# Kernel tuning notes

Measured on AMD Instinct MI355X. Metric: run time of the kernel, lower is better.

Reference implementation:

```python
import jax, jax.numpy as jnp
import numpy as np

NUM_EMBEDDINGS = 8192
EMBEDDING_DIM = 256
BETA = 0.25


def setup_inputs() -> dict:
    key = jax.random.key(0)
    k1, k2 = jax.random.split(key)
    z = jax.random.normal(k1, (16, 256, 32, 32), dtype=jnp.float32)
    # torch init: uniform(-1/K, 1/K)
    emb_w = jax.random.uniform(k2, (NUM_EMBEDDINGS, EMBEDDING_DIM),
                               dtype=jnp.float32,
                               minval=-1.0 / NUM_EMBEDDINGS,
                               maxval=1.0 / NUM_EMBEDDINGS)
    return {"z": z, "emb_w": emb_w}


def reference(z, emb_w):
    B, C, H, W = z.shape
    z_bhwc = jnp.transpose(z, (0, 2, 3, 1))          # [B,H,W,C]
    flat = z_bhwc.reshape(-1, C)                      # [N,C]
    d = (jnp.sum(flat * flat, axis=1, keepdims=True)
         + jnp.sum(emb_w * emb_w, axis=1)
         - 2.0 * flat @ emb_w.T)                      # [N,K]
    idx = jnp.argmin(d, axis=1)                       # [N]
    # direct gather (mathematically identical to one-hot @ emb_w)
    quantized = emb_w[idx].reshape(z_bhwc.shape)      # [B,H,W,C]
    q_latent_loss = jnp.mean((jax.lax.stop_gradient(quantized) - z_bhwc) ** 2)
    e_latent_loss = jnp.mean((quantized - jax.lax.stop_gradient(z_bhwc)) ** 2)
    loss = q_latent_loss + BETA * e_latent_loss
    # straight-through estimator
    quantized_st = z_bhwc + jax.lax.stop_gradient(quantized - z_bhwc)
    out = jnp.transpose(quantized_st, (0, 3, 1, 2))   # [B,C,H,W]
    return out, loss, idx.reshape(B, -1)
```

## Files before the change

### kernel.cpp

```cpp
#include <hip/hip_runtime.h>
#include <cstdint>
#include <cstddef>

#define N_PIX   16384
#define K_EMB   8192
#define DDIM    256

#define WS_A8       0
#define WS_E8       4194304
#define WS_KEYS     6291456
#define WS_ZSQ      23068672
#define WS_ESQ      23134208
#define WS_LOSS     23166976
#define WS_CNT      23166984

typedef float f32x16 __attribute__((ext_vector_type(16)));
typedef int   i32x4  __attribute__((ext_vector_type(4)));
typedef int   i32x8  __attribute__((ext_vector_type(8)));

__device__ __forceinline__ unsigned int f32_sortable(float f) {
    unsigned int u = __float_as_uint(f);
    return (u & 0x80000000u) ? ~u : (u | 0x80000000u);
}

__device__ __forceinline__ unsigned char f2fp8(float x) {
    unsigned ub = __float_as_uint(x);
    unsigned sgn = (ub >> 24) & 0x80u;
    unsigned b = ub & 0x7FFFFFFFu;
    unsigned out;
    if (__uint_as_float(b) < 0.015625f) {
        out = (unsigned)(int)rintf(__uint_as_float(b) * 512.0f);
    } else {
        unsigned r = b + 0x7FFFFu + ((b >> 20) & 1u);
        int er = (int)(r >> 23) - 127;
        out = (unsigned)(((er + 7) << 3) | ((r >> 20) & 7u));
    }
    return (unsigned char)(out | sgn);
}

#if defined(__has_builtin)
#if __has_builtin(__builtin_amdgcn_cvt_pk_fp8_f32)
#define HAVE_CVT_FP8 1
#endif
#if __has_builtin(__builtin_amdgcn_fmed3f)
#define HAVE_FMED3 1
#endif
#endif

__device__ __forceinline__ unsigned pack4_fp8(float a, float b, float c, float d) {
#ifdef HAVE_CVT_FP8
    int pk = 0;
    pk = __builtin_amdgcn_cvt_pk_fp8_f32(a, b, pk, false);
    pk = __builtin_amdgcn_cvt_pk_fp8_f32(c, d, pk, true);
    return (unsigned)pk;
#else
    return (unsigned)f2fp8(a) | ((unsigned)f2fp8(b) << 8)
         | ((unsigned)f2fp8(c) << 16) | ((unsigned)f2fp8(d) << 24);
#endif
}

__device__ __forceinline__ void async16(const unsigned char* g, unsigned char* l) {
    __builtin_amdgcn_global_load_lds(
        (const __attribute__((address_space(1))) void*)g,
        (__attribute__((address_space(3))) void*)l, 16, 0, 0);
}

__global__ __launch_bounds__(256) void prep_kernel(
        const float* __restrict__ z, const float* __restrict__ emb,
        unsigned char* __restrict__ Af8, unsigned char* __restrict__ Ef8,
        float* __restrict__ zsq, float* __restrict__ esq,
        double* __restrict__ lossAcc, unsigned* __restrict__ doneCnt) {
    __shared__ float tile[32][257];
    __shared__ float sqs[32][17];
    int blk = blockIdx.x;
    int t   = threadIdx.x;
    if (blk < 512) {
        int b   = blk >> 5;
        int hw0 = (blk & 31) * 32;
        const float* zb = z + (size_t)b * 262144 + hw0;
        int c0  = t >> 3;
        int px4 = t & 7;
#pragma unroll
        for (int cc = 0; cc < 8; ++cc) {
            int c = cc * 32 + c0;
            float4 v = *(const float4*)&zb[(size_t)c * 1024 + px4 * 4];
            tile[px4 * 4 + 0][c] = v.x;
            tile[px4 * 4 + 1][c] = v.y;
            tile[px4 * 4 + 2][c] = v.z;
            tile[px4 * 4 + 3][c] = v.w;
        }
        __syncthreads();
        int p0 = b * 1024 + hw0;
        int wv = t >> 6, lane = t & 63;
#pragma unroll
        for (int iter = 0; iter < 8; ++iter) {
            int pl = iter * 4 + wv;
            unsigned pk = pack4_fp8(tile[pl][lane * 4 + 0], tile[pl][lane * 4 + 1],
                                    tile[pl][lane * 4 + 2], tile[pl][lane * 4 + 3]);
            int p  = p0 + pl;
            int mbb = p >> 7, r = p & 127;
            int c = lane * 4;
            *(unsigned*)(Af8 + (size_t)mbb * 32768
                         + (c >> 6) * 8192 + r * 64 + (c & 63)) = pk;
        }
        {
            int row = t >> 3, s0 = t & 7;
            const float* rp = tile[row];
            float a0 = 0.f, a1 = 0.f;
#pragma unroll
            for (int i = 0; i < 16; ++i) {
                float x0 = rp[s0 + 8 * i];
                a0 = __fadd_rn(a0, __fmul_rn(x0, x0));
            }
#pragma unroll
            for (int i = 0; i < 16; ++i) {
                float x1 = rp[128 + s0 + 8 * i];
                a1 = __fadd_rn(a1, __fmul_rn(x1, x1));
            }
            sqs[row][s0]     = a0;
            sqs[row][s0 + 8] = a1;
        }
        __syncthreads();
        if (t < 32) {
            const float* r = sqs[t];
            float h0 = __fadd_rn(
                __fadd_rn(__fadd_rn(r[0], r[1]), __fadd_rn(r[2], r[3])),
                __fadd_rn(__fadd_rn(r[4], r[5]), __fadd_rn(r[6], r[7])));
            float h1 = __fadd_rn(
                __fadd_rn(__fadd_rn(r[8], r[9]), __fadd_rn(r[10], r[11])),
                __fadd_rn(__fadd_rn(r[12], r[13]), __fadd_rn(r[14], r[15])));
            zsq[p0 + t] = __fadd_rn(h0, h1);
        }
        if (blk == 0 && t == 0) { *lossAcc = 0.0; *doneCnt = 0u; }
    } else {
        int k0 = (blk - 512) * 32;
        const float4* eg = (const float4*)(emb + (size_t)k0 * DDIM);
#pragma unroll
        for (int i = 0; i < 8; ++i) {
            int idx = i * 256 + t;
            int row = idx >> 6, c4 = idx & 63;
            float4 v = eg[idx];
            *(float4*)&tile[row][c4 * 4] = v;
        }
        __syncthreads();
#pragma unroll
        for (int i = 0; i < 8; ++i) {
            int idx = i * 256 + t;
            int row = idx >> 6, c4 = idx & 63;
            const float* rp = &tile[row][c4 * 4];
            int kg = k0 + row;
            int nbb = kg >> 7, rr = kg & 127;
            int c  = c4 * 4;
            int kk = c >> 6, kl = c & 63;
            int s  = kl >> 4;
            int pos = kk * 8192 + rr * 64
                    + ((s ^ ((rr >> 1) & 3)) << 4) + (kl & 15);
            *(unsigned*)(Ef8 + (size_t)nbb * 32768 + pos) =
                pack4_fp8(rp[0] * 8192.0f, rp[1] * 8192.0f,
                          rp[2] * 8192.0f, rp[3] * 8192.0f);
        }
        {
            int row = t >> 3, s0 = t & 7;
            const float* rp = tile[row];
            float a0 = 0.f, a1 = 0.f;
#pragma unroll
            for (int i = 0; i < 16; ++i) {
                float x0 = rp[s0 + 8 * i];
                a0 = __fadd_rn(a0, __fmul_rn(x0, x0));
            }
#pragma unroll
            for (int i = 0; i < 16; ++i) {
                float x1 = rp[128 + s0 + 8 * i];
                a1 = __fadd_rn(a1, __fmul_rn(x1, x1));
            }
            sqs[row][s0]     = a0;
            sqs[row][s0 + 8] = a1;
        }
        __syncthreads();
        if (t < 32) {
            const float* r = sqs[t];
            float h0 = __fadd_rn(
                __fadd_rn(__fadd_rn(r[0], r[1]), __fadd_rn(r[2], r[3])),
                __fadd_rn(__fadd_rn(r[4], r[5]), __fadd_rn(r[6], r[7])));
            float h1 = __fadd_rn(
                __fadd_rn(__fadd_rn(r[8], r[9]), __fadd_rn(r[10], r[11])),
                __fadd_rn(__fadd_rn(r[12], r[13]), __fadd_rn(r[14], r[15])));
            esq[k0 + t] = __fadd_rn(h0, h1);
        }
    }
}

__device__ __forceinline__ unsigned pack_key(float w) {
    float uf = __builtin_fmaf(w, -512.0f, 262144.0f);
    uf = fminf(uf, 524287.0f);
    unsigned u = (unsigned)uf;
    return (u << 13) | (__float_as_uint(w) & 0x1FFFu);
}

__global__ __launch_bounds__(256) void mfma_score_kernel(
        const unsigned char* __restrict__ Af8,
        const unsigned char* __restrict__ Ef8,
        unsigned int* __restrict__ keys) {
    union __align__(16) SM {
        unsigned char Bs[2][32768];
        struct { uint2 ep[128][33]; } e;
    };
    __shared__ SM sm;

    const int g  = blockIdx.x;
    const int mb = blockIdx.y;
    const int t = threadIdx.x;
    const int w = t >> 6, lane = t & 63;
    const int wm = w >> 1, wn = w & 1;
    const int l31 = lane & 31, h = lane >> 5;

    {
        const unsigned char* Eg = Ef8 + (size_t)(g * 4) * 32768 + t * 16;
#pragma unroll
        for (int ch = 0; ch < 8; ++ch)
            async16(Eg + ch * 4096, &sm.Bs[0][ch * 4096 + t * 16]);
    }

    i32x8 afr[2][4];
    {
        const unsigned char* Ab = Af8 + (size_t)mb * 32768;
#pragma unroll
        for (int rt = 0; rt < 2; ++rt) {
            int r = wm * 64 + rt * 32 + l31;
#pragma unroll
            for (int kk = 0; kk < 4; ++kk) {
                const unsigned char* p = Ab + kk * 8192 + r * 64 + h * 32;
                i32x4 lo = *(const i32x4*)p;
                i32x4 hi = *(const i32x4*)(p + 16);
                afr[rt][kk] = __builtin_shufflevector(lo, hi,
                                                      0, 1, 2, 3, 4, 5, 6, 7);
            }
        }
    }

    const float NEGINF = __int_as_float(0xFF800000);
    float t2a[2][16], t2b[2][16];
#pragma unroll
    for (int rt = 0; rt < 2; ++rt)
#pragma unroll
        for (int q = 0; q < 16; ++q) { t2a[rt][q] = NEGINF; t2b[rt][q] = NEGINF; }

    __syncthreads();

#pragma unroll 1
    for (int j = 0; j < 4; ++j) {
        const int cur = j & 1, nxt = cur ^ 1;

        if (j < 3) {
            const unsigned char* Eg =
                Ef8 + (size_t)(g * 4 + j + 1) * 32768 + t * 16;
#pragma unroll
            for (int ch = 0; ch < 8; ++ch)
                async16(Eg + ch * 4096, &sm.Bs[nxt][ch * 4096 + t * 16]);
        }

        f32x16 acc[2][2];
#pragma unroll
        for (int rt = 0; rt < 2; ++rt)
#pragma unroll
            for (int ct = 0; ct < 2; ++ct)
#pragma unroll
                for (int q = 0; q < 16; ++q) acc[rt][ct][q] = 0.f;

#pragma unroll
        for (int kk = 0; kk < 4; ++kk) {
            i32x8 bf[2];
#pragma unroll
            for (int ct = 0; ct < 2; ++ct) {
                int c = wn * 64 + ct * 32 + l31;
                int m = (c >> 1) & 3;
                int base = kk * 8192 + c * 64;
                int s0 = h * 2;
                i32x4 lo = *(const i32x4*)
                    &sm.Bs[cur][base + ((s0 ^ m) << 4)];
                i32x4 hi = *(const i32x4*)
                    &sm.Bs[cur][base + (((s0 + 1) ^ m) << 4)];
                bf[ct] = __builtin_shufflevector(lo, hi,
                                                 0, 1, 2, 3, 4, 5, 6, 7);
            }
            __builtin_amdgcn_s_setprio(1);
#pragma unroll
            for (int rt = 0; rt < 2; ++rt)
#pragma unroll
                for (int ct = 0; ct < 2; ++ct)
                    acc[rt][ct] =
                        __builtin_amdgcn_mfma_scale_f32_32x32x64_f8f6f4(
                            afr[rt][kk], bf[ct], acc[rt][ct],
                            0, 0,
                            0, 0x7F7F7F7F,
                            0, 0x7F7F7F7F);
            __builtin_amdgcn_s_setprio(0);
        }

        const int nb = g * 4 + j;
#pragma unroll
        for (int ct = 0; ct < 2; ++ct) {
            const unsigned idxc = (unsigned)(nb * 128 + wn * 64 + ct * 32 + l31);
#pragma unroll
            for (int rt = 0; rt < 2; ++rt) {
#pragma unroll
                for (int q = 0; q < 16; ++q) {
                    float v = acc[rt][ct][q];
                    float wv = __uint_as_float(
                        (__float_as_uint(v) & 0xFFFFE000u) | idxc);
                    float a0 = t2a[rt][q], b0 = t2b[rt][q];
#ifdef HAVE_FMED3
                    float bn = __builtin_amdgcn_fmed3f(a0, wv, b0);
                    t2a[rt][q] = fmaxf(a0, wv);
                    t2b[rt][q] = bn;
#else
                    float mn = fminf(a0, wv);
                    t2a[rt][q] = fmaxf(a0, wv);
                    t2b[rt][q] = fmaxf(b0, mn);
#endif
                }
            }
        }
        __syncthreads();
    }

#pragma unroll
    for (int rt = 0; rt < 2; ++rt) {
#pragma unroll
        for (int q = 0; q < 16; ++q) {
            unsigned ka = pack_key(t2a[rt][q]);
            unsigned kb = pack_key(t2b[rt][q]);
            unsigned pa = (unsigned)__shfl_xor((int)ka, 16, 64);
            unsigned pb = (unsigned)__shfl_xor((int)kb, 16, 64);
            unsigned n0 = min(ka, pa);
            unsigned n1 = min(max(ka, pa), min(kb, pb));
            if ((lane & 16) == 0) {
                int row = wm * 64 + rt * 32 + (q & 3) + 8 * (q >> 2) + 4 * h;
                sm.e.ep[row][wn * 16 + (lane & 15)] = make_uint2(n0, n1);
            }
        }
    }
    __syncthreads();

    {
        int row = t >> 1, half = t & 1, h0 = half * 16;
        uint2 mv = sm.e.ep[row][h0];
#pragma unroll
        for (int i = 1; i < 16; ++i) {
            uint2 av = sm.e.ep[row][h0 + i];
            unsigned n0 = min(mv.x, av.x);
            unsigned n1 = min(max(mv.x, av.x), min(mv.y, av.y));
            mv.x = n0; mv.y = n1;
        }
        ((uint2*)keys)[(size_t)(g * 2 + half) * N_PIX + (mb * 128 + row)] = mv;
    }
}

__global__ __launch_bounds__(256) void final_kernel(
        const unsigned int* __restrict__ keys,
        const float* __restrict__ z, const float* __restrict__ emb,
        const float* __restrict__ zsq, const float* __restrict__ esq,
        float* __restrict__ out, float* __restrict__ idx_out,
        float* __restrict__ loss_out,
        double* __restrict__ lossAcc, unsigned* __restrict__ doneCnt) {
    __shared__ float ztile[32][257];
    __shared__ uint2 kt[32][33];
    __shared__ unsigned short scand[32][64];
    __shared__ unsigned long long ckey[2048];
    __shared__ int   soff[33];
    __shared__ int   scnt[32];
    __shared__ unsigned char pxmap[2048];
    __shared__ float szs[32];
    __shared__ int   sidx[32];

    int blk = blockIdx.x;
    int b = blk >> 5, hh2 = blk & 31;
    int t = threadIdx.x;
    int p0 = b * 1024 + hh2 * 32;
    const float* zb = z + (size_t)b * 262144 + hh2 * 32;
    {
        int c0 = t >> 3, px4 = t & 7;
#pragma unroll
        for (int cc = 0; cc < 8; ++cc) {
            int c = cc * 32 + c0;
            float4 v = *(const float4*)&zb[(size_t)c * 1024 + px4 * 4];
            ztile[px4 * 4 + 0][c] = v.x;
            ztile[px4 * 4 + 1][c] = v.y;
            ztile[px4 * 4 + 2][c] = v.z;
            ztile[px4 * 4 + 3][c] = v.w;
        }
    }
    {
        const uint2* kg = (const uint2*)keys;
#pragma unroll
        for (int itr = 0; itr < 4; ++itr) {
            int idx = itr * 256 + t;
            int px = idx & 31, hf = idx >> 5;
            kt[px][hf] = kg[(size_t)hf * N_PIX + p0 + px];
        }
    }
    if (t < 32) szs[t] = zsq[p0 + t];
    __syncthreads();

    {
        int wq = t >> 6, lane = t & 63;
#pragma unroll 1
        for (int i = 0; i < 8; ++i) {
            int px = wq * 8 + i;
            uint2 ka = (lane < 32) ? kt[px][lane] : make_uint2(~0u, ~0u);
            unsigned m = min(ka.x, ka.y);
#pragma unroll
            for (int off = 32; off >= 1; off >>= 1)
                m = min(m, (unsigned)__shfl_xor((int)m, off, 64));
            unsigned thr = (m >> 13) + 1600;

            bool h0 = (lane < 32) && ((ka.x >> 13) <= thr);
            bool h1 = (lane < 32) && ((ka.y >> 13) <= thr);
            unsigned long long m0 = __ballot(h0);
            unsigned long long m1 = __ballot(h1);
            int c0 = __popcll(m0);
            unsigned long long below = (lane == 63) ? ~0ull >> 1
                                     : ((1ull << lane) - 1);
            if (h0) scand[px][__popcll(m0 & below)] =
                (unsigned short)(ka.x & 0x1FFFu);
            if (h1) scand[px][c0 + __popcll(m1 & below)] =
                (unsigned short)(ka.y & 0x1FFFu);
            if (lane == 0) scnt[px] = c0 + __popcll(m1);
        }
    }
    __syncthreads();

    if (t < 64) {
        int v = (t < 32) ? scnt[t] : 0;
#pragma unroll
        for (int o = 1; o < 32; o <<= 1) {
            int u = __shfl_up(v, o, 64);
            if (t >= o) v += u;
        }
        if (t < 32) soff[t + 1] = v;
        if (t == 0) soff[0] = 0;
    }
    __syncthreads();
    int total = soff[32];
    for (int f = t; f < total; f += 256) {
        int lo = 0, hi = 31;
        while (lo < hi) {
            int mid = (lo + hi + 1) >> 1;
            if (soff[mid] <= f) lo = mid; else hi = mid - 1;
        }
        pxmap[f] = (unsigned char)lo;
    }
    __syncthreads();

    {
        int gid = t >> 4, l16 = t & 15;
        const float4* emb4 = (const float4*)emb;
#pragma unroll 1
        for (int f = gid; f < total; f += 16) {
            int px = pxmap[f];
            int k  = scand[px][f - soff[px]];
            double d = 0.0;
#pragma unroll
            for (int q = 0; q < 4; ++q) {
                float4 ev = emb4[(size_t)k * 64 + q * 16 + l16];
                const float* zp = &ztile[px][(q * 16 + l16) * 4];
                d += (double)zp[0] * ev.x + (double)zp[1] * ev.y
                   + (double)zp[2] * ev.z + (double)zp[3] * ev.w;
            }
#pragma unroll
            for (int o = 1; o < 16; o <<= 1) d += __shfl_xor(d, o, 64);
            if (l16 == 0) {
                float df = (float)d;
                float s  = __fsub_rn(__fadd_rn(szs[px], esq[k]),
                                     __fmul_rn(2.0f, df));
                ckey[f] = ((unsigned long long)f32_sortable(s) << 32)
                        | (unsigned)k;
            }
        }
    }
    __syncthreads();

    {
        int ci = t & 15;
#pragma unroll
        for (int pass = 0; pass < 2; ++pass) {
            int cpx = (t >> 4) + pass * 16;
            unsigned long long best = ~0ull;
            for (int f = soff[cpx] + ci; f < soff[cpx + 1]; f += 16) {
                unsigned long long v = ckey[f];
                best = v < best ? v : best;
            }
#pragma unroll
            for (int o = 1; o < 16; o <<= 1) {
                unsigned long long ov =
                    (unsigned long long)__shfl_xor((long long)best, o, 64);
                best = ov < best ? ov : best;
            }
            if (ci == 0) {
                int k = (int)(unsigned)(best & 0xffffffffu);
                sidx[cpx] = k;
                idx_out[p0 + cpx] = (float)k;
            }
        }
    }
    __syncthreads();

    int px2 = t & 31, cy = t >> 5;
    int kk = sidx[px2];
    const float* er = emb + (size_t)kk * DDIM;
    float* ob = out + (size_t)b * 262144 + hh2 * 32;
    float local = 0.f;
#pragma unroll 4
    for (int it = 0; it < 32; ++it) {
        int c = it * 8 + cy;
        float q = er[c];
        float d = q - ztile[px2][c];
        ob[(size_t)c * 1024 + px2] = q;
        local += d * d;
    }
#pragma unroll
    for (int off = 32; off >= 1; off >>= 1) local += __shfl_down(local, off, 64);
    __shared__ float wsum[4];
    if ((t & 63) == 0) wsum[t >> 6] = local;
    __syncthreads();
    if (t == 0) {
        double s = (double)wsum[0] + (double)wsum[1]
                 + (double)wsum[2] + (double)wsum[3];
        atomicAdd(lossAcc, s);
        __threadfence();
        unsigned old = atomicAdd(doneCnt, 1u);
        if (old == 511u) {
            double tot = atomicAdd(lossAcc, 0.0);
            *loss_out = (float)(tot * (1.25 / 4194304.0));
        }
    }
}

extern "C" void kernel_launch(void* const* d_in, const int* in_sizes, int n_in,
                              void* d_out, int out_size, void* d_ws, size_t ws_size,
                              hipStream_t stream) {
    const float* z   = (const float*)d_in[0];
    const float* emb = (const float*)d_in[1];
    float* out = (float*)d_out;
    char* ws = (char*)d_ws;

    unsigned char* Af8 = (unsigned char*)(ws + WS_A8);
    unsigned char* Ef8 = (unsigned char*)(ws + WS_E8);
    unsigned int* keys = (unsigned int*)(ws + WS_KEYS);
    float* zsq      = (float*)(ws + WS_ZSQ);
    float* esq      = (float*)(ws + WS_ESQ);
    double* lossAcc = (double*)(ws + WS_LOSS);
    unsigned* doneCnt = (unsigned*)(ws + WS_CNT);

    prep_kernel<<<768, 256, 0, stream>>>(z, emb, Af8, Ef8, zsq, esq,
                                         lossAcc, doneCnt);
    mfma_score_kernel<<<dim3(16, 128), 256, 0, stream>>>(Af8, Ef8, keys);
    final_kernel<<<512, 256, 0, stream>>>(keys, z, emb, zsq, esq,
                                          out, out + 4194305, out + 4194304,
                                          lossAcc, doneCnt);
}
```

Baseline: 170.3 us.

## Retile score kernel waves to 32x128 strips with a single accumulator

Each wave of the fp8 MFMA scoring kernel now owns 32 pixel rows by 128 codebook columns, instead of a 64x64 tile in a 2x2 wave grid. This halves the A fragments held in registers and keeps one accumulator live at a time instead of four, cutting register pressure so occupancy can rise. Because each wave now covers all 128 columns, the cross-lane shuffle merge of top-2 candidates is dropped. The cost is twice as much codebook B data read from LDS per wave, and shorter independent MFMA chains for hiding latency.

```diff
diff --git a/kernel.cpp b/kernel.cpp
--- a/kernel.cpp
+++ b/kernel.cpp
@@ -211,7 +211,6 @@
     const int mb = blockIdx.y;
     const int t = threadIdx.x;
     const int w = t >> 6, lane = t & 63;
-    const int wm = w >> 1, wn = w & 1;
     const int l31 = lane & 31, h = lane >> 5;
 
     {
@@ -221,29 +220,23 @@
             async16(Eg + ch * 4096, &sm.Bs[0][ch * 4096 + t * 16]);
     }
 
-    i32x8 afr[2][4];
+    i32x8 afr[4];
     {
         const unsigned char* Ab = Af8 + (size_t)mb * 32768;
-#pragma unroll
-        for (int rt = 0; rt < 2; ++rt) {
-            int r = wm * 64 + rt * 32 + l31;
-#pragma unroll
-            for (int kk = 0; kk < 4; ++kk) {
-                const unsigned char* p = Ab + kk * 8192 + r * 64 + h * 32;
-                i32x4 lo = *(const i32x4*)p;
-                i32x4 hi = *(const i32x4*)(p + 16);
-                afr[rt][kk] = __builtin_shufflevector(lo, hi,
-                                                      0, 1, 2, 3, 4, 5, 6, 7);
-            }
+        int r = w * 32 + l31;
+#pragma unroll
+        for (int kk = 0; kk < 4; ++kk) {
+            const unsigned char* p = Ab + kk * 8192 + r * 64 + h * 32;
+            i32x4 lo = *(const i32x4*)p;
+            i32x4 hi = *(const i32x4*)(p + 16);
+            afr[kk] = __builtin_shufflevector(lo, hi, 0, 1, 2, 3, 4, 5, 6, 7);
         }
     }
 
     const float NEGINF = __int_as_float(0xFF800000);
-    float t2a[2][16], t2b[2][16];
-#pragma unroll
-    for (int rt = 0; rt < 2; ++rt)
-#pragma unroll
-        for (int q = 0; q < 16; ++q) { t2a[rt][q] = NEGINF; t2b[rt][q] = NEGINF; }
+    float t2a[16], t2b[16];
+#pragma unroll
+    for (int q = 0; q < 16; ++q) { t2a[q] = NEGINF; t2b[q] = NEGINF; }
 
     __syncthreads();
 
@@ -259,86 +252,59 @@
                 async16(Eg + ch * 4096, &sm.Bs[nxt][ch * 4096 + t * 16]);
         }
 
-        f32x16 acc[2][2];
-#pragma unroll
-        for (int rt = 0; rt < 2; ++rt)
-#pragma unroll
-            for (int ct = 0; ct < 2; ++ct)
-#pragma unroll
-                for (int q = 0; q < 16; ++q) acc[rt][ct][q] = 0.f;
-
-#pragma unroll
-        for (int kk = 0; kk < 4; ++kk) {
-            i32x8 bf[2];
-#pragma unroll
-            for (int ct = 0; ct < 2; ++ct) {
-                int c = wn * 64 + ct * 32 + l31;
-                int m = (c >> 1) & 3;
+        const int nb = g * 4 + j;
+#pragma unroll
+        for (int ct = 0; ct < 4; ++ct) {
+            f32x16 acc;
+#pragma unroll
+            for (int q = 0; q < 16; ++q) acc[q] = 0.f;
+
+            const int c  = ct * 32 + l31;
+            const int m  = (c >> 1) & 3;
+            const int s0 = h * 2;
+            __builtin_amdgcn_s_setprio(1);
+#pragma unroll
+            for (int kk = 0; kk < 4; ++kk) {
                 int base = kk * 8192 + c * 64;
-                int s0 = h * 2;
                 i32x4 lo = *(const i32x4*)
                     &sm.Bs[cur][base + ((s0 ^ m) << 4)];
                 i32x4 hi = *(const i32x4*)
                     &sm.Bs[cur][base + (((s0 + 1) ^ m) << 4)];
-                bf[ct] = __builtin_shufflevector(lo, hi,
-                                                 0, 1, 2, 3, 4, 5, 6, 7);
-            }
-            __builtin_amdgcn_s_setprio(1);
-#pragma unroll
-            for (int rt = 0; rt < 2; ++rt)
-#pragma unroll
-                for (int ct = 0; ct < 2; ++ct)
-                    acc[rt][ct] =
-                        __builtin_amdgcn_mfma_scale_f32_32x32x64_f8f6f4(
-                            afr[rt][kk], bf[ct], acc[rt][ct],
-                            0, 0,
-                            0, 0x7F7F7F7F,
-                            0, 0x7F7F7F7F);
+                i32x8 bf = __builtin_shufflevector(lo, hi,
+                                                   0, 1, 2, 3, 4, 5, 6, 7);
+                acc = __builtin_amdgcn_mfma_scale_f32_32x32x64_f8f6f4(
+                        afr[kk], bf, acc,
+                        0, 0,
+                        0, 0x7F7F7F7F,
+                        0, 0x7F7F7F7F);
+            }
             __builtin_amdgcn_s_setprio(0);
-        }
-
-        const int nb = g * 4 + j;
-#pragma unroll
-        for (int ct = 0; ct < 2; ++ct) {
-            const unsigned idxc = (unsigned)(nb * 128 + wn * 64 + ct * 32 + l31);
-#pragma unroll
-            for (int rt = 0; rt < 2; ++rt) {
-#pragma unroll
-                for (int q = 0; q < 16; ++q) {
-                    float v = acc[rt][ct][q];
-                    float wv = __uint_as_float(
-                        (__float_as_uint(v) & 0xFFFFE000u) | idxc);
-                    float a0 = t2a[rt][q], b0 = t2b[rt][q];
+
+            const unsigned idxc = (unsigned)(nb * 128 + c);
+#pragma unroll
+            for (int q = 0; q < 16; ++q) {
+                float v = acc[q];
+                float wv = __uint_as_float(
+                    (__float_as_uint(v) & 0xFFFFE000u) | idxc);
+                float a0 = t2a[q], b0 = t2b[q];
 #ifdef HAVE_FMED3
-                    float bn = __builtin_amdgcn_fmed3f(a0, wv, b0);
-                    t2a[rt][q] = fmaxf(a0, wv);
-                    t2b[rt][q] = bn;
+                float bn = __builtin_amdgcn_fmed3f(a0, wv, b0);
+                t2a[q] = fmaxf(a0, wv);
+                t2b[q] = bn;
 #else
-                    float mn = fminf(a0, wv);
-                    t2a[rt][q] = fmaxf(a0, wv);
-                    t2b[rt][q] = fmaxf(b0, mn);
+                float mn = fminf(a0, wv);
+                t2a[q] = fmaxf(a0, wv);
+                t2b[q] = fmaxf(b0, mn);
 #endif
-                }
             }
         }
         __syncthreads();
     }
 
 #pragma unroll
-    for (int rt = 0; rt < 2; ++rt) {
-#pragma unroll
-        for (int q = 0; q < 16; ++q) {
-            unsigned ka = pack_key(t2a[rt][q]);
-            unsigned kb = pack_key(t2b[rt][q]);
-            unsigned pa = (unsigned)__shfl_xor((int)ka, 16, 64);
-            unsigned pb = (unsigned)__shfl_xor((int)kb, 16, 64);
-            unsigned n0 = min(ka, pa);
-            unsigned n1 = min(max(ka, pa), min(kb, pb));
-            if ((lane & 16) == 0) {
-                int row = wm * 64 + rt * 32 + (q & 3) + 8 * (q >> 2) + 4 * h;
-                sm.e.ep[row][wn * 16 + (lane & 15)] = make_uint2(n0, n1);
-            }
-        }
+    for (int q = 0; q < 16; ++q) {
+        int row = w * 32 + (q & 3) + 8 * (q >> 2) + 4 * h;
+        sm.e.ep[row][l31] = make_uint2(pack_key(t2a[q]), pack_key(t2b[q]));
     }
     __syncthreads();
 
```

Result: faster. 164.2 us (-3.5%).
